# Optimization experiments

Hardware: AMD Instinct MI355X
Metric: run time of the kernel (lower is better)

Reference implementation:

```python
import jax, jax.numpy as jnp
import numpy as np
from jax import lax

B, T, D = 2, 2048, 2048
H = 8
DK = D // H          # head_qk_dim = 256 (expand_k forced to 1.0)
DV = D // H          # head_v_dim = 256 (expand_v forced to 1.0)
CONV_K = 4
CHUNK = 64
EPS = 1e-5
INTER = 2816         # int(2048*2*2/3)=2730 -> round up to multiple of 256


def setup_inputs() -> dict:
    key = jax.random.key(0)
    ks = jax.random.split(key, 14)
    s = 0.02
    return {
        "hidden_states": jax.random.normal(ks[0], (B, T, D), jnp.float32),
        "attn_norm_w": jnp.ones((D,), jnp.float32),
        "Wq": jax.random.normal(ks[1], (D, D), jnp.float32) * s,
        "Wk": jax.random.normal(ks[2], (D, D), jnp.float32) * s,
        "Wv": jax.random.normal(ks[3], (D, D), jnp.float32) * s,
        "Wg": jax.random.normal(ks[4], (D, D), jnp.float32) * s,
        "Wo": jax.random.normal(ks[5], (D, D), jnp.float32) * s,
        "conv_wq": jax.random.normal(ks[6], (D, CONV_K), jnp.float32) * 0.3,
        "conv_wk": jax.random.normal(ks[7], (D, CONV_K), jnp.float32) * 0.3,
        "conv_wv": jax.random.normal(ks[8], (D, CONV_K), jnp.float32) * 0.3,
        "gnorm_w": jnp.ones((DV,), jnp.float32),
        "mlp_norm_w": jnp.ones((D,), jnp.float32),
        "W_gate": jax.random.normal(ks[9], (D, 2 * INTER), jnp.float32) * s,
        "W_down": jax.random.normal(ks[10], (INTER, D), jnp.float32) * s,
    }


def rmsnorm(x, w, eps=EPS):
    return x * lax.rsqrt(jnp.mean(x * x, axis=-1, keepdims=True) + eps) * w


def short_conv_silu(x, w):
    # depthwise causal conv1d, kernel CONV_K, no bias, then SiLU. x: [B,T,C], w: [C,K]
    K = w.shape[-1]
    xp = jnp.pad(x, ((0, 0), (K - 1, 0), (0, 0)))
    y = sum(xp[:, i:i + x.shape[1], :] * w[None, None, :, i] for i in range(K))
    return jax.nn.silu(y)


def rope(x, cos, sin):
    # non-interleaved (GPT-NeoX style) rotary over full head dim. x: [B,T,H,d]
    x1, x2 = jnp.split(x, 2, axis=-1)
    c = cos[None, :, None, :]
    s = sin[None, :, None, :]
    return jnp.concatenate([x1 * c - x2 * s, x2 * c + x1 * s], axis=-1)


def chunk_retention(q, k, v, gamma, C=CHUNK):
    # q,k,v: [B,T,H,d]; gamma: [H]. o_t = q_t @ S_t, S_t = gamma*S_{t-1} + k_t^T v_t
    b, t, h, dk = q.shape
    dv = v.shape[-1]
    q = q * (dk ** -0.5)
    n = t // C
    to_chunks = lambda x: x.reshape(b, n, C, h, -1).transpose(1, 0, 3, 2, 4)  # [n,B,H,C,d]
    qc, kc, vc = map(to_chunks, (q, k, v))
    i = jnp.arange(C)
    diff = i[:, None] - i[None, :]
    pe = jnp.where(diff >= 0, diff, 0).astype(q.dtype)
    Dm = jnp.where(diff >= 0, gamma[:, None, None] ** pe, 0.0)       # [H,C,C] intra-chunk decay
    di = gamma[:, None] ** (i + 1).astype(q.dtype)                    # [H,C] decay from prev state
    dkc = gamma[:, None] ** (C - 1 - i).astype(q.dtype)               # [H,C] decay to chunk end
    gC = gamma ** C                                                   # [H]

    def step(S, xs):
        qi, ki, vi = xs                                              # [B,H,C,d]
        A = jnp.einsum('bhid,bhjd->bhij', qi, ki) * Dm
        o = A @ vi + jnp.einsum('bhid,bhde->bhie', qi, S) * di[None, :, :, None]
        S = S * gC[None, :, None, None] + jnp.einsum('bhjd,bhje->bhde', ki * dkc[None, :, :, None], vi)
        return S, o

    S0 = jnp.zeros((b, h, dk, dv), q.dtype)
    _, oc = lax.scan(step, S0, (qc, kc, vc))                          # [n,B,H,C,dv]
    return oc.transpose(1, 0, 3, 2, 4).reshape(b, t, h, dv)


def reference(hidden_states, attn_norm_w, Wq, Wk, Wv, Wg, Wo,
              conv_wq, conv_wk, conv_wv, gnorm_w, mlp_norm_w, W_gate, W_down):
    b, t, d = hidden_states.shape
    # --- MultiScaleRetention block (pre-norm) ---
    x = rmsnorm(hidden_states, attn_norm_w)
    q = short_conv_silu(x @ Wq, conv_wq)
    k = short_conv_silu(x @ Wk, conv_wk)
    v = short_conv_silu(x @ Wv, conv_wv)
    q = q.reshape(b, t, H, DK)
    k = k.reshape(b, t, H, DK)
    v = v.reshape(b, t, H, DV)
    # rotary embedding (base 10000), seqlen_offset=0
    inv_freq = 1.0 / (10000.0 ** (jnp.arange(0, DK, 2, dtype=jnp.float32) / DK))
    freqs = jnp.arange(t, dtype=jnp.float32)[:, None] * inv_freq[None, :]   # [T,DK/2]
    cos, sin = jnp.cos(freqs), jnp.sin(freqs)
    q, k = rope(q, cos, sin), rope(k, cos, sin)
    # per-head retention decay: gamma_h = 1 - 2^(-5-h)
    gamma = 1.0 - jnp.exp2(-5.0 - jnp.arange(H, dtype=jnp.float32))
    o = chunk_retention(q, k, v, gamma)                                     # [B,T,H,DV]
    # fused RMSNorm + swish gate
    g = (x @ Wg).reshape(b, t, H, DV)
    o = rmsnorm(o, gnorm_w) * (g * jax.nn.sigmoid(g))
    o = o.reshape(b, t, d) @ Wo
    h = hidden_states + o
    # --- gated MLP block (pre-norm, SwiGLU) ---
    y = rmsnorm(h, mlp_norm_w)
    gy = y @ W_gate
    gate, yv = jnp.split(gy, 2, axis=-1)
    y = (gate * jax.nn.sigmoid(gate) * yv) @ W_down
    return h + y
```

## Files before the change

kernel.cpp:

```cpp
#include <hip/hip_runtime.h>
#include <hip/hip_bf16.h>
#include <cstdint>
#include <cstddef>
#include <type_traits>


typedef __hip_bfloat16 bf16;
typedef __bf16 bf16x8 __attribute__((ext_vector_type(8)));
typedef __bf16 bf16x4 __attribute__((ext_vector_type(4)));
typedef float f32x4 __attribute__((ext_vector_type(4)));

#define DEVI __device__ __forceinline__

DEVI float bf2f(bf16 x) { return __bfloat162float(x); }
DEVI bf16 f2bf(float x) { return __float2bfloat16(x); }
DEVI float siluf(float x) { return x / (1.f + __expf(-x)); }
DEVI float log2gamma(int h) {
  return log1pf(-exp2f(-5.f - (float)h)) * 1.4426950408889634f;
}

#define GLL16(gp, lp)                                                  \
  __builtin_amdgcn_global_load_lds(                                    \
      (__attribute__((address_space(1))) void*)(gp),                   \
      (__attribute__((address_space(3))) void*)(lp), 16, 0, 0)

DEVI float blockSum256(float v) {
  #pragma unroll
  for (int off = 32; off; off >>= 1) v += __shfl_down(v, off, 64);
  __shared__ float sm[4];
  int lane = threadIdx.x & 63, w = threadIdx.x >> 6;
  if (lane == 0) sm[w] = v;
  __syncthreads();
  return sm[0] + sm[1] + sm[2] + sm[3];
}

__global__ void rmsnorm_k(const float* __restrict__ x, const float* __restrict__ w,
                          bf16* __restrict__ out) {
  long row = blockIdx.x;
  const float* xr = x + row * 2048;
  int i0 = threadIdx.x * 4;
  float4 v0 = *(const float4*)(xr + i0);
  float4 v1 = *(const float4*)(xr + 1024 + i0);
  float ss = v0.x*v0.x + v0.y*v0.y + v0.z*v0.z + v0.w*v0.w
           + v1.x*v1.x + v1.y*v1.y + v1.z*v1.z + v1.w*v1.w;
  ss = blockSum256(ss);
  float s = rsqrtf(ss * (1.f/2048.f) + 1e-5f);
  bf16* orow = out + row * 2048;
  orow[i0+0] = f2bf(v0.x*s*w[i0+0]); orow[i0+1] = f2bf(v0.y*s*w[i0+1]);
  orow[i0+2] = f2bf(v0.z*s*w[i0+2]); orow[i0+3] = f2bf(v0.w*s*w[i0+3]);
  orow[1024+i0+0] = f2bf(v1.x*s*w[1024+i0+0]); orow[1024+i0+1] = f2bf(v1.y*s*w[1024+i0+1]);
  orow[1024+i0+2] = f2bf(v1.z*s*w[1024+i0+2]); orow[1024+i0+3] = f2bf(v1.w*s*w[1024+i0+3]);
}

__global__ void rope_init(float2* __restrict__ tab) {
  int t = blockIdx.x, j = threadIdx.x;
  double inv = exp((double)(-j) * (9.210340371976184 / 128.0));
  double ang = fmod((double)t * inv, 6.283185307179586);
  tab[t * 128 + j] = make_float2((float)cos(ang), (float)sin(ang));
}

__global__ void transpose_w(const float* __restrict__ in, bf16* __restrict__ out,
                            int R, int C) {
  __shared__ float tile[32][33];
  int bx = blockIdx.x * 32, by = blockIdx.y * 32;
  int tx = threadIdx.x, ty = threadIdx.y;
  #pragma unroll
  for (int i = 0; i < 32; i += 8)
    tile[ty + i][tx] = in[(long)(by + ty + i) * C + bx + tx];
  __syncthreads();
  #pragma unroll
  for (int i = 0; i < 32; i += 8)
    out[(long)(bx + ty + i) * R + by + tx] = f2bf(tile[tx][ty + i]);
}

__global__ void transpose_w4(const float* __restrict__ w0, const float* __restrict__ w1,
                             const float* __restrict__ w2, const float* __restrict__ w3,
                             bf16* __restrict__ out) {
  __shared__ float tile[32][33];
  const float* in = blockIdx.z == 0 ? w0 : blockIdx.z == 1 ? w1
                   : blockIdx.z == 2 ? w2 : w3;
  int bx = blockIdx.x * 32, by = blockIdx.y * 32;
  int tx = threadIdx.x, ty = threadIdx.y;
  #pragma unroll
  for (int i = 0; i < 32; i += 8)
    tile[ty + i][tx] = in[(long)(by + ty + i) * 2048 + bx + tx];
  __syncthreads();
  long rbase = (long)blockIdx.z * 2048;
  #pragma unroll
  for (int i = 0; i < 32; i += 8)
    out[(rbase + bx + ty + i) * 2048 + by + tx] = f2bf(tile[tx][ty + i]);
}

__global__ void transpose_wgate(const float* __restrict__ in, bf16* __restrict__ out) {
  __shared__ float tile[32][33];
  int bx = blockIdx.x * 32, by = blockIdx.y * 32;
  int tx = threadIdx.x, ty = threadIdx.y;
  int r = bx + tx;
  int gidx = r >> 4;
  int scol = ((gidx & 1) ? 2816 : 0) + ((gidx >> 1) << 4) + (r & 15);
  #pragma unroll
  for (int i = 0; i < 32; i += 8)
    tile[ty + i][tx] = in[(long)(by + ty + i) * 5632 + scol];
  __syncthreads();
  #pragma unroll
  for (int i = 0; i < 32; i += 8)
    out[(long)(bx + ty + i) * 2048 + by + tx] = f2bf(tile[tx][ty + i]);
}

__global__ void transpose_head(const bf16* __restrict__ in, bf16* __restrict__ out,
                               int withDecay) {
  __shared__ bf16 tile[32][33];
  const int bh = blockIdx.z, hh = bh & 7;
  const float lg = log2gamma(hh);
  const int t0 = blockIdx.y * 32, d0 = blockIdx.x * 32;
  const int tx = threadIdx.x, ty = threadIdx.y;
  const bf16* src = in + (long)bh * 2048 * 256;
  bf16* dst = out + (long)bh * 2048 * 256;
  #pragma unroll
  for (int i = 0; i < 32; i += 8) {
    int t = t0 + ty + i;
    float v = bf2f(src[(long)t * 256 + d0 + tx]);
    if (withDecay) v *= exp2f(lg * (float)(63 - (t & 63)));
    tile[ty + i][tx] = f2bf(v);
  }
  __syncthreads();
  #pragma unroll
  for (int i = 0; i < 32; i += 8)
    dst[(long)(d0 + ty + i) * 2048 + t0 + tx] = tile[tx][ty + i];
}

template <typename OUT_T, bool DO_ADD, bool DO_SWIGLU>
__global__ __launch_bounds__(256) void gemm_bt(
    const bf16* __restrict__ A, const bf16* __restrict__ Bt,
    OUT_T* __restrict__ C, int ldc, bf16* __restrict__ C2, int split,
    const float* __restrict__ addend, int M, int N, int K) {
  __shared__ alignas(16) bf16 As[128 * 64];
  __shared__ alignas(16) bf16 Bs[128 * 64];
  const int tid = threadIdx.x;
  const int lane = tid & 63, wid = tid >> 6;
  const int quad = lane >> 4, l16 = lane & 15;
  const int wm = wid >> 1, wn = wid & 1;
  const long bm = (long)blockIdx.x * 128;
  const long bn = (long)blockIdx.y * 128;

  const int srow = wid * 8 + (lane >> 3);
  const int scb = lane & 7;
  const int scbG = scb ^ (lane >> 3);
  const bf16* pa[4]; const bf16* pb[4]; bf16* la[4]; bf16* lb[4];
  #pragma unroll
  for (int c = 0; c < 4; c++) {
    int row = c * 32 + srow;
    pa[c] = A + (bm + row) * (long)K + scbG * 8;
    pb[c] = Bt + (bn + row) * (long)K + scbG * 8;
    la[c] = As + row * 64 + scb * 8;
    lb[c] = Bs + row * 64 + scb * 8;
  }

  const f32x4 zz = {0.f, 0.f, 0.f, 0.f};
  f32x4 acc[4][4];
  #pragma unroll
  for (int i = 0; i < 4; i++)
    #pragma unroll
    for (int j = 0; j < 4; j++) acc[i][j] = zz;

  const int l7 = l16 & 7;
  for (int k0 = 0; k0 < K; k0 += 64) {
    #pragma unroll
    for (int c = 0; c < 4; c++) {
      GLL16(pa[c] + k0, la[c]);
      GLL16(pb[c] + k0, lb[c]);
    }
    __syncthreads();
    #pragma unroll
    for (int ks = 0; ks < 2; ks++) {
      const int fcol = ((ks * 4 + quad) ^ l7) * 8;
      bf16x8 a[4], b[4];
      #pragma unroll
      for (int i = 0; i < 4; i++)
        a[i] = *(const bf16x8*)(As + (wm * 64 + i * 16 + l16) * 64 + fcol);
      #pragma unroll
      for (int j = 0; j < 4; j++)
        b[j] = *(const bf16x8*)(Bs + (wn * 64 + j * 16 + l16) * 64 + fcol);
      #pragma unroll
      for (int i = 0; i < 4; i++)
        #pragma unroll
        for (int j = 0; j < 4; j++)
          acc[i][j] = __builtin_amdgcn_mfma_f32_16x16x32_bf16(a[i], b[j], acc[i][j], 0, 0, 0);
    }
    __syncthreads();
  }

  if constexpr (DO_SWIGLU) {
    #pragma unroll
    for (int i = 0; i < 4; i++)
      #pragma unroll
      for (int jp = 0; jp < 2; jp++) {
        long acol = bn / 2 + wn * 32 + jp * 16 + l16;
        #pragma unroll
        for (int r = 0; r < 4; r++) {
          long row = bm + wm * 64 + i * 16 + quad * 4 + r;
          float gate = acc[i][2 * jp][r];
          float val = acc[i][2 * jp + 1][r];
          C2[row * 2816 + acol] = f2bf(siluf(gate) * val);
        }
      }
  } else {
    const bool sec = (bn >= split);
    #pragma unroll
    for (int i = 0; i < 4; i++)
      #pragma unroll
      for (int j = 0; j < 4; j++)
        #pragma unroll
        for (int r = 0; r < 4; r++) {
          long row = bm + wm * 64 + i * 16 + quad * 4 + r;
          long col = bn + wn * 64 + j * 16 + l16;
          float v = acc[i][j][r];
          if (sec) {
            C2[row * 2048 + (col - split)] = f2bf(v);
          } else {
            if constexpr (DO_ADD) v += addend[row * (long)ldc + col];
            if constexpr (std::is_same<OUT_T, float>::value)
              C[row * (long)ldc + col] = v;
            else
              C[row * (long)ldc + col] = f2bf(v);
          }
        }
  }
}

__global__ void conv3(const bf16* __restrict__ u3,
                      const float* __restrict__ cwq, const float* __restrict__ cwk,
                      const float* __restrict__ cwv, const float2* __restrict__ rtab,
                      bf16* __restrict__ qb, bf16* __restrict__ kb,
                      bf16* __restrict__ vb) {
  const int bt = blockIdx.x;
  const int t = bt & 2047;
  const int b = bt >> 11;
  const int z = blockIdx.y;
  const int tid = threadIdx.x;
  const int h = tid >> 5;
  if (z < 2) {
    const float* cw = z == 0 ? cwq : cwk;
    bf16* out = z == 0 ? qb : kb;
    const float scale = z == 0 ? 0.0625f : 1.0f;
    const int j0 = (tid & 31) * 4;
    const int ch1 = h * 256 + j0, ch2 = ch1 + 128;
    const int c1 = z * 2048 + ch1, c2 = c1 + 128;
    f32x4 w1[4], w2[4];
    #pragma unroll
    for (int e = 0; e < 4; e++) {
      w1[e] = *(const f32x4*)(cw + (ch1 + e) * 4);
      w2[e] = *(const f32x4*)(cw + (ch2 + e) * 4);
    }
    float a1[4] = {0.f, 0.f, 0.f, 0.f}, a2[4] = {0.f, 0.f, 0.f, 0.f};
    #pragma unroll
    for (int i = 0; i < 4; i++) {
      int ts = t - 3 + i;
      if (ts >= 0) {
        const bf16* up = u3 + (long)(bt - 3 + i) * 6144;
        bf16x4 v1 = *(const bf16x4*)(up + c1);
        bf16x4 v2 = *(const bf16x4*)(up + c2);
        #pragma unroll
        for (int e = 0; e < 4; e++) {
          a1[e] += (float)v1[e] * w1[e][i];
          a2[e] += (float)v2[e] * w2[e][i];
        }
      }
    }
    f32x4 r01 = *(const f32x4*)(rtab + t * 128 + j0);
    f32x4 r23 = *(const f32x4*)(rtab + t * 128 + j0 + 2);
    float cs[4] = {r01[0], r01[2], r23[0], r23[2]};
    float sn[4] = {r01[1], r01[3], r23[1], r23[3]};
    bf16x4 o1, o2;
    #pragma unroll
    for (int e = 0; e < 4; e++) {
      float s1 = siluf(a1[e]), s2 = siluf(a2[e]);
      o1[e] = (__bf16)((s1 * cs[e] - s2 * sn[e]) * scale);
      o2[e] = (__bf16)((s2 * cs[e] + s1 * sn[e]) * scale);
    }
    long obase = ((long)(b * 8 + h) * 2048 + t) * 256;
    *(bf16x4*)(out + obase + j0) = o1;
    *(bf16x4*)(out + obase + 128 + j0) = o2;
  } else {
    const int e0 = (tid & 31) * 8;
    const int ch = h * 256 + e0;
    const int c = 4096 + ch;
    f32x4 w[8];
    #pragma unroll
    for (int e = 0; e < 8; e++) w[e] = *(const f32x4*)(cwv + (ch + e) * 4);
    float a[8] = {0.f, 0.f, 0.f, 0.f, 0.f, 0.f, 0.f, 0.f};
    #pragma unroll
    for (int i = 0; i < 4; i++) {
      int ts = t - 3 + i;
      if (ts >= 0) {
        bf16x8 v = *(const bf16x8*)(u3 + (long)(bt - 3 + i) * 6144 + c);
        #pragma unroll
        for (int e = 0; e < 8; e++) a[e] += (float)v[e] * w[e][i];
      }
    }
    bf16x8 o;
    #pragma unroll
    for (int e = 0; e < 8; e++) o[e] = (__bf16)siluf(a[e]);
    *(bf16x8*)(vb + ((long)(b * 8 + h) * 2048 + t) * 256 + e0) = o;
  }
}

__global__ __launch_bounds__(256) void chunk_outer(
    const bf16* __restrict__ vT, const bf16* __restrict__ kTd,
    bf16* __restrict__ states) {
  __shared__ alignas(16) bf16 lk[256 * 72];
  const int chunk = blockIdx.x, bh = blockIdx.y;
  const int tid = threadIdx.x;
  const int lane = tid & 63, wid = tid >> 6;
  const int quad = lane >> 4, l16 = lane & 15;
  const long base = (long)bh * 256 * 2048 + chunk * 64;

  #pragma unroll
  for (int it = 0; it < 8; it++) {
    int r = it * 32 + (tid >> 3);
    int cb = tid & 7;
    *(int4*)(lk + r * 72 + cb * 8) = *(const int4*)(kTd + base + (long)r * 2048 + cb * 8);
  }
  bf16x8 a[4][2];
  #pragma unroll
  for (int i = 0; i < 4; i++)
    #pragma unroll
    for (int ks = 0; ks < 2; ks++)
      a[i][ks] = *(const bf16x8*)(vT + base + (long)(wid * 64 + i * 16 + l16) * 2048 +
                                  ks * 32 + quad * 8);
  __syncthreads();

  bf16* sout = states + ((long)bh * 32 + chunk) * 65536;
  const f32x4 zz = {0.f, 0.f, 0.f, 0.f};
  for (int g = 0; g < 4; g++) {
    f32x4 acc[4][4];
    #pragma unroll
    for (int i = 0; i < 4; i++)
      #pragma unroll
      for (int j = 0; j < 4; j++) acc[i][j] = zz;
    #pragma unroll
    for (int ks = 0; ks < 2; ks++) {
      bf16x8 b[4];
      #pragma unroll
      for (int j = 0; j < 4; j++)
        b[j] = *(const bf16x8*)(lk + (g * 64 + j * 16 + l16) * 72 + ks * 32 + quad * 8);
      #pragma unroll
      for (int i = 0; i < 4; i++)
        #pragma unroll
        for (int j = 0; j < 4; j++)
          acc[i][j] = __builtin_amdgcn_mfma_f32_16x16x32_bf16(a[i][ks], b[j], acc[i][j], 0, 0, 0);
    }
    #pragma unroll
    for (int i = 0; i < 4; i++)
      #pragma unroll
      for (int j = 0; j < 4; j++)
        #pragma unroll
        for (int r = 0; r < 4; r++) {
          int e = wid * 64 + i * 16 + quad * 4 + r;
          int d = g * 64 + j * 16 + l16;
          sout[(long)e * 256 + d] = f2bf(acc[i][j][r]);
        }
  }
}

__global__ void state_scan(bf16* __restrict__ states) {
  const int bh = blockIdx.y, h = bh & 7;
  const float gC = exp2f(64.f * log2gamma(h));
  long idx = ((long)blockIdx.x * 256 + threadIdx.x) * 8;
  bf16* p = states + (long)bh * 32 * 65536 + idx;
  float s[8] = {0.f, 0.f, 0.f, 0.f, 0.f, 0.f, 0.f, 0.f};
  for (int n = 0; n < 32; n++) {
    bf16x8 m = *(const bf16x8*)(p + (long)n * 65536);
    bf16x8 o;
    #pragma unroll
    for (int e = 0; e < 8; e++) {
      o[e] = (__bf16)s[e];
      s[e] = gC * s[e] + (float)m[e];
    }
    *(bf16x8*)(p + (long)n * 65536) = o;
  }
}

__global__ __launch_bounds__(256) void chunk_inner(
    const bf16* __restrict__ q, const bf16* __restrict__ k,
    const bf16* __restrict__ vT, const bf16* __restrict__ ST,
    const bf16* __restrict__ g, const float* __restrict__ gw,
    bf16* __restrict__ og) {
  __shared__ alignas(16) bf16 P[64 * 328];
  __shared__ float sq[64][4];
  __shared__ float sscale[64];
  const int chunk = blockIdx.x, bh = blockIdx.y;
  const int b_ = bh >> 3, h = bh & 7;
  const float lg = log2gamma(h);
  const int tid = threadIdx.x;
  const int lane = tid & 63, wid = tid >> 6;
  const int quad = lane >> 4, l16 = lane & 15;
  const long qkbase = ((long)bh * 2048 + chunk * 64) * 256;

  {
    const int row = tid >> 2, cb = tid & 3;
    const float di = exp2f(lg * (float)(row + 1));
    const bf16* qs = q + qkbase + (long)row * 256 + cb * 64;
    bf16* pd = P + row * 328 + 64 + cb * 64;
    #pragma unroll
    for (int mb = 0; mb < 8; mb++) {
      bf16x8 v = *(const bf16x8*)(qs + mb * 8);
      #pragma unroll
      for (int e = 0; e < 8; e++) pd[mb * 8 + e] = f2bf((float)v[e] * di);
    }
  }

  {
    const f32x4 zz = {0.f, 0.f, 0.f, 0.f};
    f32x4 acc[4];
    #pragma unroll
    for (int j = 0; j < 4; j++) acc[j] = zz;
    #pragma unroll
    for (int ks = 0; ks < 8; ks++) {
      bf16x8 a = *(const bf16x8*)(q + qkbase + (long)(wid * 16 + l16) * 256 + ks * 32 + quad * 8);
      #pragma unroll
      for (int j = 0; j < 4; j++) {
        bf16x8 b = *(const bf16x8*)(k + qkbase + (long)(j * 16 + l16) * 256 + ks * 32 + quad * 8);
        acc[j] = __builtin_amdgcn_mfma_f32_16x16x32_bf16(a, b, acc[j], 0, 0, 0);
      }
    }
    #pragma unroll
    for (int j = 0; j < 4; j++)
      #pragma unroll
      for (int r = 0; r < 4; r++) {
        int il = wid * 16 + quad * 4 + r;
        int jl = j * 16 + l16;
        int dd = il - jl;
        float v = (dd >= 0) ? acc[j][r] * exp2f(lg * (float)dd) : 0.f;
        P[il * 328 + jl] = f2bf(v);
      }
  }
  __syncthreads();

  const f32x4 zz = {0.f, 0.f, 0.f, 0.f};
  f32x4 acc[4][4];
  #pragma unroll
  for (int i = 0; i < 4; i++)
    #pragma unroll
    for (int j = 0; j < 4; j++) acc[i][j] = zz;
  const long vbase = (long)bh * 256 * 2048 + chunk * 64;
  const long sbase = ((long)bh * 32 + chunk) * 65536;
  #pragma unroll
  for (int ks = 0; ks < 10; ks++) {
    bf16x8 a[4];
    #pragma unroll
    for (int i = 0; i < 4; i++)
      a[i] = *(const bf16x8*)(P + (i * 16 + l16) * 328 + ks * 32 + quad * 8);
    int kk = ks * 32 + quad * 8;
    bf16x8 b[4];
    #pragma unroll
    for (int j = 0; j < 4; j++) {
      int e = wid * 64 + j * 16 + l16;
      const bf16* src = (kk < 64) ? (vT + vbase + (long)e * 2048 + kk)
                                  : (ST + sbase + (long)e * 256 + (kk - 64));
      b[j] = *(const bf16x8*)src;
    }
    #pragma unroll
    for (int i = 0; i < 4; i++)
      #pragma unroll
      for (int j = 0; j < 4; j++)
        acc[i][j] = __builtin_amdgcn_mfma_f32_16x16x32_bf16(a[i], b[j], acc[i][j], 0, 0, 0);
  }

  #pragma unroll
  for (int i = 0; i < 4; i++)
    #pragma unroll
    for (int r = 0; r < 4; r++) {
      float s = acc[i][0][r]*acc[i][0][r] + acc[i][1][r]*acc[i][1][r]
              + acc[i][2][r]*acc[i][2][r] + acc[i][3][r]*acc[i][3][r];
      s += __shfl_xor(s, 1, 64);
      s += __shfl_xor(s, 2, 64);
      s += __shfl_xor(s, 4, 64);
      s += __shfl_xor(s, 8, 64);
      if (l16 == 0) sq[i * 16 + quad * 4 + r][wid] = s;
    }
  __syncthreads();
  if (tid < 64) {
    float t = sq[tid][0] + sq[tid][1] + sq[tid][2] + sq[tid][3];
    sscale[tid] = rsqrtf(t * (1.f/256.f) + 1e-5f);
  }
  __syncthreads();

  #pragma unroll
  for (int i = 0; i < 4; i++)
    #pragma unroll
    for (int j = 0; j < 4; j++) {
      int e = wid * 64 + j * 16 + l16;
      float w = gw[e];
      #pragma unroll
      for (int r = 0; r < 4; r++) {
        int row = i * 16 + quad * 4 + r;
        long bt = (long)b_ * 2048 + chunk * 64 + row;
        float gg = bf2f(g[bt * 2048 + h * 256 + e]);
        float val = acc[i][j][r] * sscale[row] * w * siluf(gg);
        og[bt * 2048 + h * 256 + e] = f2bf(val);
      }
    }
}

extern "C" void kernel_launch(void* const* d_in, const int* in_sizes, int n_in,
                              void* d_out, int out_size, void* d_ws, size_t ws_size,
                              hipStream_t stream) {
  (void)in_sizes; (void)n_in; (void)out_size;
  const float* hidden = (const float*)d_in[0];
  const float* attn_w = (const float*)d_in[1];
  const float* Wq = (const float*)d_in[2];
  const float* Wk = (const float*)d_in[3];
  const float* Wv = (const float*)d_in[4];
  const float* Wg = (const float*)d_in[5];
  const float* Wo = (const float*)d_in[6];
  const float* cwq = (const float*)d_in[7];
  const float* cwk = (const float*)d_in[8];
  const float* cwv = (const float*)d_in[9];
  const float* gnw = (const float*)d_in[10];
  const float* mlpw = (const float*)d_in[11];
  const float* Wgate = (const float*)d_in[12];
  const float* Wdown = (const float*)d_in[13];
  float* out = (float*)d_out;
  char* ws = (char*)d_ws;

  if (ws_size < 209715200ull) return;

  const size_t MB16 = 16777216ull;
  char* WTr = ws;
  bf16* WT4    = (bf16*)WTr;
  bf16* kTb    = (bf16*)WTr;
  bf16* WoT    = (bf16*)WTr;
  bf16* WgateT = (bf16*)WTr;
  bf16* WdownT = (bf16*)WTr;
  bf16* og     = (bf16*)(WTr + MB16);
  char* Ur = ws + 33554432ull;
  bf16*  u3     = (bf16*)Ur;
  bf16*  xbf    = (bf16*)(Ur + 50331648ull);
  bf16*  states = (bf16*)Ur;
  float* hbuf   = (float*)Ur;
  bf16*  act    = (bf16*)(Ur + 33554432ull);
  char* Qr = ws + 100663296ull;
  bf16* qb  = (bf16*)Qr;
  bf16* kb  = (bf16*)(Qr + MB16);
  bf16* vTb = (bf16*)(Qr + 2 * MB16);
  bf16* vnb = (bf16*)(Qr + 3 * MB16);
  bf16* ybf = (bf16*)(Qr + 50331648ull);
  bf16* g   = (bf16*)(ws + 167772160ull);
  float2* rtab = (float2*)(ws + 184549376ull);

  dim3 tb32(32, 8);

  rope_init<<<2048, 128, 0, stream>>>(rtab);
  rmsnorm_k<<<4096, 256, 0, stream>>>(hidden, attn_w, xbf);

  transpose_w4<<<dim3(64, 64, 4), tb32, 0, stream>>>(Wq, Wk, Wv, Wg, WT4);
  gemm_bt<bf16, false, false><<<dim3(32, 64), 256, 0, stream>>>(
      xbf, WT4, u3, 6144, g, 6144, nullptr, 4096, 8192, 2048);

  conv3<<<dim3(4096, 3), 256, 0, stream>>>(u3, cwq, cwk, cwv, rtab, qb, kb, vnb);
  transpose_head<<<dim3(8, 64, 16), tb32, 0, stream>>>(kb, kTb, 1);
  transpose_head<<<dim3(8, 64, 16), tb32, 0, stream>>>(vnb, vTb, 0);

  chunk_outer<<<dim3(32, 16), 256, 0, stream>>>(vTb, kTb, states);
  state_scan<<<dim3(32, 16), 256, 0, stream>>>(states);
  chunk_inner<<<dim3(32, 16), 256, 0, stream>>>(qb, kb, vTb, states, g, gnw, og);

  transpose_w<<<dim3(64, 64), tb32, 0, stream>>>(Wo, WoT, 2048, 2048);
  gemm_bt<float, true, false><<<dim3(32, 16), 256, 0, stream>>>(
      og, WoT, hbuf, 2048, nullptr, 1 << 30, hidden, 4096, 2048, 2048);

  rmsnorm_k<<<4096, 256, 0, stream>>>(hbuf, mlpw, ybf);
  transpose_wgate<<<dim3(176, 64), tb32, 0, stream>>>(Wgate, WgateT);
  gemm_bt<bf16, false, true><<<dim3(32, 44), 256, 0, stream>>>(
      ybf, WgateT, nullptr, 2816, act, 1 << 30, nullptr, 4096, 5632, 2048);
  transpose_w<<<dim3(64, 88), tb32, 0, stream>>>(Wdown, WdownT, 2816, 2048);
  gemm_bt<float, true, false><<<dim3(32, 16), 256, 0, stream>>>(
      act, WdownT, out, 2048, nullptr, 1 << 30, hbuf, 4096, 2048, 2816);
}
```

Measured before the change: 786.1 us.

## Add 256x256-tile 8-wave pipelined GEMM for QKVG and gate projections

Measured after the change: 799.2 us. About the same (+1.7%).

```diff
diff --git a/kernel.cpp b/kernel.cpp
--- a/kernel.cpp
+++ b/kernel.cpp
@@ -226,6 +226,182 @@
           }
         }
   }
+}
+
+#define BAR() __builtin_amdgcn_s_barrier()
+#define LGKM0() asm volatile("s_waitcnt lgkmcnt(0)" ::: "memory")
+#define VMW(n) asm volatile("s_waitcnt vmcnt(" #n ")" ::: "memory")
+
+template <typename OUT_T, bool DO_SWIGLU>
+__global__ __launch_bounds__(512, 2) void gemm256(
+    const bf16* __restrict__ A, const bf16* __restrict__ Bt,
+    OUT_T* __restrict__ C, int ldc, bf16* __restrict__ C2, int split,
+    int M, int N, int K) {
+  __shared__ alignas(16) bf16 As[2][256 * 64];
+  __shared__ alignas(16) bf16 Bs[2][256 * 64];
+  const int tid = threadIdx.x;
+  const int lane = tid & 63, wid = tid >> 6;
+  const int quad = lane >> 4, l16 = lane & 15, l7 = l16 & 7;
+  const int wm = wid >> 2, wn = wid & 3;
+  const long bm = (long)blockIdx.x * 256;
+  const long bn = (long)blockIdx.y * 256;
+  const int NT = K >> 6;
+
+  const int srow8 = lane >> 3;
+  const int sgr = lane & 7;
+  const int sgrG = sgr ^ srow8;
+  const int arow = wid * 8 + srow8;
+  const int brow = (wid & 3) * 8 + srow8 + (wid >> 2) * 64;
+
+#define STAGE_A(bufi, kt, base) do {                                         \
+    int r0_ = (base) + arow, r1_ = r0_ + 128;                                \
+    GLL16(A + (bm + r0_) * (long)K + (kt) * 64 + sgrG * 8,                   \
+          &As[bufi][r0_ * 64 + sgr * 8]);                                    \
+    GLL16(A + (bm + r1_) * (long)K + (kt) * 64 + sgrG * 8,                   \
+          &As[bufi][r1_ * 64 + sgr * 8]);                                    \
+  } while (0)
+#define STAGE_B(bufi, kt, base) do {                                         \
+    int r0_ = (base) + brow, r1_ = r0_ + 128;                                \
+    GLL16(Bt + (bn + r0_) * (long)K + (kt) * 64 + sgrG * 8,                  \
+          &Bs[bufi][r0_ * 64 + sgr * 8]);                                    \
+    GLL16(Bt + (bn + r1_) * (long)K + (kt) * 64 + sgrG * 8,                  \
+          &Bs[bufi][r1_ * 64 + sgr * 8]);                                    \
+  } while (0)
+
+#define LDA(bufi, mh) do {                                                   \
+    _Pragma("unroll")                                                        \
+    for (int mi = 0; mi < 4; mi++) {                                         \
+      const bf16* p_ = &As[bufi][(wm * 128 + ((mh) * 4 + mi) * 16 + l16) * 64]; \
+      afr[mi][0] = *(const bf16x8*)(p_ + ((quad ^ l7) * 8));                 \
+      afr[mi][1] = *(const bf16x8*)(p_ + (((4 + quad) ^ l7) * 8));           \
+    } } while (0)
+#define LDB(bufi, nh) do {                                                   \
+    _Pragma("unroll")                                                        \
+    for (int ni = 0; ni < 2; ni++) {                                         \
+      const bf16* p_ = &Bs[bufi][(wn * 64 + ((nh) * 2 + ni) * 16 + l16) * 64]; \
+      bq[ni][0] = *(const bf16x8*)(p_ + ((quad ^ l7) * 8));                  \
+      bq[ni][1] = *(const bf16x8*)(p_ + (((4 + quad) ^ l7) * 8));            \
+    } } while (0)
+#define MFMAQ(mh, nh) do {                                                   \
+    __builtin_amdgcn_s_setprio(1);                                           \
+    _Pragma("unroll")                                                        \
+    for (int ks = 0; ks < 2; ks++)                                           \
+      _Pragma("unroll")                                                      \
+      for (int mi = 0; mi < 4; mi++)                                         \
+        _Pragma("unroll")                                                    \
+        for (int ni = 0; ni < 2; ni++)                                       \
+          acc[(mh) * 4 + mi][(nh) * 2 + ni] =                                \
+              __builtin_amdgcn_mfma_f32_16x16x32_bf16(                       \
+                  afr[mi][ks], bq[ni][ks],                                   \
+                  acc[(mh) * 4 + mi][(nh) * 2 + ni], 0, 0, 0);               \
+    __builtin_amdgcn_s_setprio(0);                                           \
+  } while (0)
+
+  const f32x4 zz = {0.f, 0.f, 0.f, 0.f};
+  f32x4 acc[8][4];
+  #pragma unroll
+  for (int i = 0; i < 8; i++)
+    #pragma unroll
+    for (int j = 0; j < 4; j++) acc[i][j] = zz;
+
+  STAGE_B(0, 0, 0);
+  STAGE_A(0, 0, 64);
+  STAGE_A(0, 0, 0);
+  STAGE_B(0, 0, 32);
+  STAGE_B(1, 1, 0);
+  STAGE_A(1, 1, 64);
+  VMW(6);
+  BAR();
+
+  bf16x8 afr[4][2], bq[2][2];
+  for (int T = 0; T < NT; T += 2) {
+    const bool more = (T + 2 < NT);
+    LDA(0, 0); LDB(0, 0);
+    STAGE_A(1, T + 1, 0);
+    BAR();
+    MFMAQ(0, 0);
+    LGKM0(); BAR();
+    LDA(0, 1);
+    STAGE_B(1, T + 1, 32);
+    VMW(8);
+    BAR();
+    MFMAQ(1, 0);
+    LGKM0(); BAR();
+    LDB(0, 1);
+    if (more) STAGE_B(0, T + 2, 0);
+    BAR();
+    MFMAQ(1, 1);
+    LGKM0(); BAR();
+    LDA(0, 0);
+    if (more) STAGE_A(0, T + 2, 64);
+    if (more) { VMW(6); } else { VMW(2); }
+    BAR();
+    MFMAQ(0, 1);
+    LGKM0(); BAR();
+    LDA(1, 0); LDB(1, 0);
+    if (more) STAGE_A(0, T + 2, 0);
+    BAR();
+    MFMAQ(0, 0);
+    LGKM0(); BAR();
+    LDA(1, 1);
+    if (more) STAGE_B(0, T + 2, 32);
+    if (more) { VMW(8); } else { VMW(0); }
+    BAR();
+    MFMAQ(1, 0);
+    LGKM0(); BAR();
+    LDB(1, 1);
+    if (more) STAGE_B(1, T + 3, 0);
+    BAR();
+    MFMAQ(1, 1);
+    LGKM0(); BAR();
+    LDA(1, 0);
+    if (more) STAGE_A(1, T + 3, 64);
+    if (more) VMW(6);
+    BAR();
+    MFMAQ(0, 1);
+    LGKM0(); BAR();
+  }
+
+  if constexpr (DO_SWIGLU) {
+    #pragma unroll
+    for (int mf = 0; mf < 8; mf++)
+      #pragma unroll
+      for (int jp = 0; jp < 2; jp++) {
+        long acol = bn / 2 + wn * 32 + jp * 16 + l16;
+        #pragma unroll
+        for (int r = 0; r < 4; r++) {
+          long row = bm + wm * 128 + mf * 16 + quad * 4 + r;
+          float gate = acc[mf][2 * jp][r];
+          float val = acc[mf][2 * jp + 1][r];
+          C2[row * 2816 + acol] = f2bf(siluf(gate) * val);
+        }
+      }
+  } else {
+    const bool sec = (bn >= split);
+    #pragma unroll
+    for (int mf = 0; mf < 8; mf++)
+      #pragma unroll
+      for (int nf = 0; nf < 4; nf++)
+        #pragma unroll
+        for (int r = 0; r < 4; r++) {
+          long row = bm + wm * 128 + mf * 16 + quad * 4 + r;
+          long col = bn + wn * 64 + nf * 16 + l16;
+          float v = acc[mf][nf][r];
+          if (sec) {
+            C2[row * 2048 + (col - split)] = f2bf(v);
+          } else {
+            if constexpr (std::is_same<OUT_T, float>::value)
+              C[row * (long)ldc + col] = v;
+            else
+              C[row * (long)ldc + col] = f2bf(v);
+          }
+        }
+  }
+#undef STAGE_A
+#undef STAGE_B
+#undef LDA
+#undef LDB
+#undef MFMAQ
 }
 
 __global__ void conv3(const bf16* __restrict__ u3,
@@ -555,8 +731,8 @@
   rmsnorm_k<<<4096, 256, 0, stream>>>(hidden, attn_w, xbf);
 
   transpose_w4<<<dim3(64, 64, 4), tb32, 0, stream>>>(Wq, Wk, Wv, Wg, WT4);
-  gemm_bt<bf16, false, false><<<dim3(32, 64), 256, 0, stream>>>(
-      xbf, WT4, u3, 6144, g, 6144, nullptr, 4096, 8192, 2048);
+  gemm256<bf16, false><<<dim3(16, 32), 512, 0, stream>>>(
+      xbf, WT4, u3, 6144, g, 6144, 4096, 8192, 2048);
 
   conv3<<<dim3(4096, 3), 256, 0, stream>>>(u3, cwq, cwk, cwv, rtab, qb, kb, vnb);
   transpose_head<<<dim3(8, 64, 16), tb32, 0, stream>>>(kb, kTb, 1);
@@ -572,8 +748,8 @@
 
   rmsnorm_k<<<4096, 256, 0, stream>>>(hbuf, mlpw, ybf);
   transpose_wgate<<<dim3(176, 64), tb32, 0, stream>>>(Wgate, WgateT);
-  gemm_bt<bf16, false, true><<<dim3(32, 44), 256, 0, stream>>>(
-      ybf, WgateT, nullptr, 2816, act, 1 << 30, nullptr, 4096, 5632, 2048);
+  gemm256<bf16, true><<<dim3(16, 22), 512, 0, stream>>>(
+      ybf, WgateT, (bf16*)nullptr, 0, act, 1 << 30, 4096, 5632, 2048);
   transpose_w<<<dim3(64, 88), tb32, 0, stream>>>(Wdown, WdownT, 2816, 2048);
   gemm_bt<float, true, false><<<dim3(32, 16), 256, 0, stream>>>(
       act, WdownT, out, 2048, nullptr, 1 << 30, hbuf, 4096, 2048, 2816);
```
